# Kernel tuning notes

Hardware: AMD Instinct MI355X
Metric: run time of the kernel (lower is better)

Reference implementation:

```python
import jax, jax.numpy as jnp
import numpy as np

B, L, D, H = 8, 2048, 1024, 2048


def setup_inputs() -> dict:
    key = jax.random.key(0)
    ks = jax.random.split(key, 4)
    hidden = jax.random.normal(ks[0], (B, L, D), dtype=jnp.float32)
    lengths = jax.random.randint(ks[1], (B,), L // 2, L + 1)
    attention_mask = (jnp.arange(L)[None, :] < lengths[:, None]).astype(jnp.float32)
    target_boundary_counts = lengths.astype(jnp.float32) / 8.0
    W1 = jax.random.normal(ks[2], (D, H), dtype=jnp.float32) * (1.0 / np.sqrt(D))
    b1 = jnp.zeros((H,), jnp.float32)
    W2 = jax.random.normal(ks[3], (H, 1), dtype=jnp.float32) * (1.0 / np.sqrt(H))
    b2 = jnp.full((1,), -2.5, jnp.float32)  # init_for_12 bias fill
    return dict(hidden=hidden, attention_mask=attention_mask,
                target_boundary_counts=target_boundary_counts,
                W1=W1, b1=b1, W2=W2, b2=b2)


def sinusoidal_pos_emb(S, d, dtype):
    pos = jnp.arange(S, dtype=jnp.float32)[:, None]
    i = jnp.arange(0, d, 2, dtype=jnp.float32)[None, :]
    ang = pos / jnp.power(10000.0, i / d)
    pe = jnp.zeros((S, d), jnp.float32)
    pe = pe.at[:, 0::2].set(jnp.sin(ang))
    pe = pe.at[:, 1::2].set(jnp.cos(ang))
    return pe.astype(dtype)


def downsample(boundaries, hidden, mask):
    # boundaries: (B,L) straight-through; hidden: (B,L,D); mask: (B,L)
    # segment id of token t = cumsum(b)[t] - b[t]; mean-pool tokens per segment.
    # S is padded to L (static shape); unused trailing segments pool to zero.
    hh1 = jnp.cumsum(boundaries, axis=1) - boundaries            # (B,L)
    foo = jnp.arange(L, dtype=boundaries.dtype)[None, None, :] - hh1[:, :, None]  # (B,L,S)
    sel = jax.lax.stop_gradient(foo) == 0
    lel = jnp.where(sel, 1.0 - foo, 0.0)                          # straight-through weights
    lel = lel * mask[:, :, None]
    lel = lel / (jnp.sum(lel, axis=1, keepdims=True) + 1e-9)
    return jnp.einsum('bld,bls->bsd', hidden, lel)                # (B,S,D)


def reference(hidden, attention_mask, target_boundary_counts, W1, b1, W2, b2):
    # eval mode: dropout is identity, soft_boundaries = probs
    logits = (jax.nn.relu(hidden @ W1 + b1) @ W2 + b2)[..., 0]    # (B,L)
    probs = jax.nn.sigmoid(logits)
    hard = (probs > 0.5).astype(jnp.float32)
    hb = hard + probs - jax.lax.stop_gradient(probs)              # straight-through
    hb = hb * attention_mask
    # force a boundary at the last real token of each padded sequence
    pad = attention_mask == 0
    first_pad = pad & (jnp.cumsum(pad.astype(jnp.int32), axis=1) == 1)
    last_real = jnp.roll(first_pad, -1, axis=1).at[:, -1].set(False)
    hb = jnp.maximum(hb, last_real.astype(jnp.float32))

    pooled = downsample(hb, hidden, attention_mask)               # (B,S=L,D)
    pooled = pooled + sinusoidal_pos_emb(pooled.shape[1], D, pooled.dtype)[None]

    counts = jnp.sum(jax.lax.stop_gradient(hb), axis=1)           # boundaries per item
    shortened_attention_mask = (jnp.arange(L, dtype=jnp.float32)[None, :] < counts[:, None]).astype(jnp.float32)

    # per-item binomial NLL against p = target_count / length, mean over batch, x10
    n = jnp.sum(attention_mask, axis=1)
    k = jnp.sum(hb, axis=1)
    p = jnp.clip(target_boundary_counts / jnp.clip(n, 1.0, None), 1e-6, 1.0 - 1e-6)
    log_prob = (jax.lax.lgamma(n + 1.0) - jax.lax.lgamma(k + 1.0)
                - jax.lax.lgamma(n - k + 1.0)
                + k * jnp.log(p) + (n - k) * jnp.log1p(-p))
    loss = 10.0 * jnp.mean(-log_prob)

    num_boundaries = jnp.sum(hb)
    total_positions = jnp.sum(attention_mask)
    return pooled, loss, num_boundaries, total_positions, shortened_attention_mask
```

## Files before the change

### kernel.cpp

```cpp
#include <hip/hip_runtime.h>
#include <math.h>

#define B_   8
#define L_   2048
#define D_   1024
#define H_   2048
#define NBLK 8
#define CHK  32
#define NCH  (L_ / CHK)
#define BK   64
#define NK   (D_ / BK)
#define MARGIN  0.5f
#define MAXFLAG 1024
#define BSCALE  16.0f
#define BUNSCALE 0.0625f

typedef __bf16 bf16_t;
typedef float  f32x4_t  __attribute__((ext_vector_type(4)));
typedef int    i32x4_t  __attribute__((ext_vector_type(4)));
typedef long   i64x2_t  __attribute__((ext_vector_type(2)));

#define TILE_BYTES 16384

__device__ inline int pk4_fp8(float a, float b, float c, float d) {
  int w = __builtin_amdgcn_cvt_pk_fp8_f32(a, b, 0, false);
  w = __builtin_amdgcn_cvt_pk_fp8_f32(c, d, w, true);
  return w;
}

__global__ __launch_bounds__(256) void k0_pack(
    const float* __restrict__ A,
    const float* __restrict__ W1,
    unsigned char* __restrict__ Abf,
    unsigned char* __restrict__ Bbf,
    float* __restrict__ chunkSum,
    int* __restrict__ flagcnt)
{
  __shared__ float scratch[256][33];
  const int kt = blockIdx.x;
  const int yy = blockIdx.y;
  const int r  = threadIdx.x;

  if (yy >= 64) {
    const int nt = yy - 64;
    if (kt == 0 && nt == 0 && r == 0) *flagcnt = 0;
    const float* src = W1 + (size_t)(kt * BK) * H_ + nt * 256 + r;
    float v[64];
#pragma unroll
    for (int j = 0; j < 64; ++j) v[j] = src[(size_t)j * H_] * BSCALE;
    char* dst = (char*)Bbf + ((size_t)(nt * 16 + kt)) * TILE_BYTES + r * 64;
#pragma unroll
    for (int g = 0; g < 4; ++g) {
      i32x4_t o;
      o[0] = pk4_fp8(v[g*8+0], v[g*8+1], v[g*8+2], v[g*8+3]);
      o[1] = pk4_fp8(v[g*8+4], v[g*8+5], v[g*8+6], v[g*8+7]);
      o[2] = pk4_fp8(v[32+g*8+0], v[32+g*8+1], v[32+g*8+2], v[32+g*8+3]);
      o[3] = pk4_fp8(v[32+g*8+4], v[32+g*8+5], v[32+g*8+6], v[32+g*8+7]);
      *(i32x4_t*)(dst + ((g ^ ((r >> 1) & 3)) << 4)) = o;
    }
    return;
  }

  const int mt = yy;
  const float* src = A + (size_t)(mt * 256 + r) * D_ + kt * BK;
  float v[64];
#pragma unroll
  for (int q = 0; q < 16; ++q) {
    f32x4_t x = *(const f32x4_t*)(src + q * 4);
    v[q*4] = x.x; v[q*4+1] = x.y; v[q*4+2] = x.z; v[q*4+3] = x.w;
  }
  char* dst = (char*)Abf + ((size_t)(mt * 16 + kt)) * TILE_BYTES + r * 64;
#pragma unroll
  for (int g = 0; g < 4; ++g) {
    i32x4_t o;
    o[0] = pk4_fp8(v[g*8+0], v[g*8+1], v[g*8+2], v[g*8+3]);
    o[1] = pk4_fp8(v[g*8+4], v[g*8+5], v[g*8+6], v[g*8+7]);
    o[2] = pk4_fp8(v[32+g*8+0], v[32+g*8+1], v[32+g*8+2], v[32+g*8+3]);
    o[3] = pk4_fp8(v[32+g*8+4], v[32+g*8+5], v[32+g*8+6], v[32+g*8+7]);
    *(i32x4_t*)(dst + ((g ^ ((r >> 1) & 3)) << 4)) = o;
  }
  const int ch = r >> 5, j = r & 31;
  const int b  = mt >> 3;
  const int cg = (mt & 7) * 8 + ch;
#pragma unroll
  for (int half = 0; half < 2; ++half) {
    __syncthreads();
#pragma unroll
    for (int q = 0; q < 8; ++q)
      *(f32x4_t*)&scratch[r][q * 4] = *(const f32x4_t*)&v[half * 32 + q * 4];
    __syncthreads();
    float s = 0.f;
#pragma unroll
    for (int q = 0; q < 32; ++q) s += scratch[ch * 32 + q][j];
    chunkSum[((size_t)(b * NCH + cg)) * D_ + kt * BK + half * 32 + j] = s;
  }
}

__global__ __launch_bounds__(512, 2) void k1_gemm(
    const unsigned char* __restrict__ Abf,
    const unsigned char* __restrict__ Bbf,
    const float* __restrict__ b1,
    const float* __restrict__ W2,
    float* __restrict__ partial)
{
  extern __shared__ __align__(16) unsigned char lds[];

  const int tid  = threadIdx.x;
  const int wg   = (blockIdx.x & 7) * 64 + (blockIdx.x >> 3);
  const int mt   = wg >> 3;
  const int nt   = wg & 7;
  const int m0   = mt * 256;
  const int n0   = nt * 256;
  const int lane = tid & 63;
  const int wave = tid >> 6;
  const int wr = wave >> 2, wc = wave & 3;
  const int lr = lane & 15, lk = lane >> 4;

  const char* aT = (const char*)Abf + ((size_t)mt * NK) * TILE_BYTES;
  const char* bT = (const char*)Bbf + ((size_t)nt * NK) * TILE_BYTES;

  f32x4_t acc[8][4];
#pragma unroll
  for (int m = 0; m < 8; ++m)
#pragma unroll
    for (int n = 0; n < 4; ++n)
      acc[m][n] = (f32x4_t){0.f, 0.f, 0.f, 0.f};

  auto stage = [&](int t, int buf) {
    const char* ga = aT + (size_t)t * TILE_BYTES;
    const char* gb = bT + (size_t)t * TILE_BYTES;
    unsigned char* lb = lds + buf * 32768;
#pragma unroll
    for (int j = 0; j < 4; ++j) {
      const int i = j * 512 + tid;
      const char* g = (j < 2) ? ga + i * 16 : gb + (i - 1024) * 16;
      __builtin_amdgcn_global_load_lds(
          (const __attribute__((address_space(1))) void*)g,
          (__attribute__((address_space(3))) void*)(lb + i * 16),
          16, 0, 0);
    }
  };

  stage(0, 0);
  stage(1, 1);
  for (int t = 0; t < NK; ++t) {
    if (t + 2 < NK) {
      stage(t + 2, (t + 2) & 3);
      asm volatile("s_waitcnt vmcnt(8)" ::: "memory");
    } else if (t + 1 < NK) {
      asm volatile("s_waitcnt vmcnt(4)" ::: "memory");
    } else {
      asm volatile("s_waitcnt vmcnt(0)" ::: "memory");
    }
    __builtin_amdgcn_s_barrier();
    asm volatile("" ::: "memory");

    const char* sA = (const char*)(lds + (t & 3) * 32768);
    const char* sB = sA + 16384;
    i64x2_t a[8], b[4];
#pragma unroll
    for (int m = 0; m < 8; ++m) {
      const int r = wr * 128 + m * 16 + lr;
      a[m] = *(const i64x2_t*)(sA + r * 64 + ((lk ^ ((r >> 1) & 3)) << 4));
    }
#pragma unroll
    for (int n = 0; n < 4; ++n) {
      const int c = wc * 64 + n * 16 + lr;
      b[n] = *(const i64x2_t*)(sB + c * 64 + ((lk ^ ((c >> 1) & 3)) << 4));
    }
#pragma unroll
    for (int m = 0; m < 8; ++m)
#pragma unroll
      for (int n = 0; n < 4; ++n)
        acc[m][n] = __builtin_amdgcn_mfma_f32_16x16x32_fp8_fp8(
            a[m].x, b[n].x, acc[m][n], 0, 0, 0);
#pragma unroll
    for (int m = 0; m < 8; ++m)
#pragma unroll
      for (int n = 0; n < 4; ++n)
        acc[m][n] = __builtin_amdgcn_mfma_f32_16x16x32_fp8_fp8(
            a[m].y, b[n].y, acc[m][n], 0, 0, 0);
  }

  float rs[8][4];
#pragma unroll
  for (int m = 0; m < 8; ++m)
#pragma unroll
    for (int rg = 0; rg < 4; ++rg) rs[m][rg] = 0.f;

#pragma unroll
  for (int n = 0; n < 4; ++n) {
    const int jg = n0 + wc * 64 + n * 16 + lr;
    const float w2v = W2[jg];
    const float b1v = b1[jg];
#pragma unroll
    for (int m = 0; m < 8; ++m)
#pragma unroll
      for (int rg = 0; rg < 4; ++rg) {
        float v = acc[m][n][rg] * BUNSCALE + b1v;
        rs[m][rg] += fmaxf(v, 0.f) * w2v;
      }
  }
#pragma unroll
  for (int m = 0; m < 8; ++m)
#pragma unroll
    for (int rg = 0; rg < 4; ++rg) {
      float v = rs[m][rg];
      v += __shfl_xor(v, 1);
      v += __shfl_xor(v, 2);
      v += __shfl_xor(v, 4);
      v += __shfl_xor(v, 8);
      rs[m][rg] = v;
    }
  __syncthreads();
  float (*part_lds)[4] = (float(*)[4])lds;
  if (lr == 0) {
#pragma unroll
    for (int m = 0; m < 8; ++m)
#pragma unroll
      for (int rg = 0; rg < 4; ++rg)
        part_lds[wr * 128 + m * 16 + lk * 4 + rg][wc] = rs[m][rg];
  }
  __syncthreads();
  if (tid < 256) {
    const float sum = part_lds[tid][0] + part_lds[tid][1]
                    + part_lds[tid][2] + part_lds[tid][3];
    partial[(size_t)(m0 + tid) * NBLK + nt] = sum;
  }
}

__global__ __launch_bounds__(256) void k2a_logits(
    const float* __restrict__ partial,
    const float* __restrict__ b2,
    float* __restrict__ logits,
    int* __restrict__ flaglist,
    int* __restrict__ flagcnt)
{
  const int i = blockIdx.x * 256 + threadIdx.x;
  const float* pp = partial + (size_t)i * NBLK;
  float lg = b2[0];
#pragma unroll
  for (int j = 0; j < NBLK; ++j) lg += pp[j];
  logits[i] = lg;
  if (fabsf(lg) < MARGIN) {
    int s = atomicAdd(flagcnt, 1);
    if (s < MAXFLAG) flaglist[s] = i;
  }
}

__global__ __launch_bounds__(256) void k2b_fixup(
    const float* __restrict__ hidden,
    const float* __restrict__ W1,
    const float* __restrict__ b1,
    const float* __restrict__ W2,
    const int* __restrict__ flaglist,
    const int* __restrict__ flagcnt,
    float* __restrict__ fixpart)
{
  const int cnt = min(*flagcnt, MAXFLAG);
  const int cg = blockIdx.x;
  __shared__ float hrow[D_];
  __shared__ float red[256];
  const int tid = threadIdx.x;
  const int col = cg * 256 + tid;
  for (int f = blockIdx.y; f < cnt; f += 64) {
    const int i = flaglist[f];
    const float* h = hidden + (size_t)i * D_;
    __syncthreads();
    *(f32x4_t*)&hrow[tid * 4] = *(const f32x4_t*)&h[tid * 4];
    __syncthreads();
    float acc = 0.f;
#pragma unroll 8
    for (int k = 0; k < D_; ++k)
      acc = fmaf(hrow[k], W1[(size_t)k * H_ + col], acc);
    red[tid] = fmaxf(acc + b1[col], 0.f) * W2[col];
    __syncthreads();
    for (int st = 128; st > 0; st >>= 1) {
      if (tid < st) red[tid] += red[tid + st];
      __syncthreads();
    }
    if (tid == 0) fixpart[f * 8 + cg] = red[0];
  }
}

__global__ __launch_bounds__(256) void k2c_scan(
    float* __restrict__ logits,
    const float* __restrict__ mask,
    const float* __restrict__ target,
    const float* __restrict__ b2,
    const float* __restrict__ fixpart,
    const int* __restrict__ flaglist,
    const int* __restrict__ flagcnt,
    float* __restrict__ outmask,
    int*   __restrict__ seg,
    float* __restrict__ hdr)
{
  const int b = blockIdx.x, tid = threadIdx.x;
  __shared__ float redf[256];
  __shared__ int tsum[256];
  __shared__ unsigned char hbs[L_];

  const int cnt = min(*flagcnt, MAXFLAG);
  for (int f = tid; f < cnt; f += 256) {
    const int i = flaglist[f];
    if ((i >> 11) == b) {
      float s = b2[0];
#pragma unroll
      for (int cg = 0; cg < 8; ++cg) s += fixpart[f * 8 + cg];
      logits[i] = s;
    }
  }
  float lm = 0.f;
#pragma unroll
  for (int e = 0; e < 8; ++e) lm += mask[b * L_ + tid * 8 + e];
  redf[tid] = lm;
  __syncthreads();
  for (int s = 128; s > 0; s >>= 1) {
    if (tid < s) redf[tid] += redf[tid + s];
    __syncthreads();
  }
  const int length = (int)(redf[0] + 0.5f);

  int hloc[8];
  int lsum = 0;
#pragma unroll
  for (int e = 0; e < 8; ++e) {
    const int t = tid * 8 + e;
    const float lg = logits[b * L_ + t];
    int hb = (lg > 0.f) && (t < length);
    if (length < L_ && t == length - 1) hb = 1;
    hloc[e] = hb;
    hbs[t] = (unsigned char)hb;
    lsum += hb;
  }
  tsum[tid] = lsum;
  __syncthreads();
  for (int off = 1; off < 256; off <<= 1) {
    int v = tsum[tid];
    int add = (tid >= off) ? tsum[tid - off] : 0;
    __syncthreads();
    tsum[tid] = v + add;
    __syncthreads();
  }
  const int ktot = tsum[255];

  int pre = tsum[tid] - lsum;
  for (int e = 0; e < 8; ++e) {
    const int t = tid * 8 + e;
    if (t < length) {
      const bool st = (t == 0) || hbs[t - 1];
      if (st) seg[b * 2050 + pre] = t;
    }
    pre += hloc[e];
  }

#pragma unroll
  for (int e = 0; e < 8; ++e) {
    const int t = tid * 8 + e;
    outmask[b * L_ + t] = (t < ktot) ? 1.f : 0.f;
  }

  __syncthreads();
  if (tid == 0) {
    const int maxseg = ktot - (length > 0 ? (int)hbs[length - 1] : 0);
    seg[b * 2050 + maxseg + 1] = length;
    const float n = (float)length, k = (float)ktot;
    float p = target[b] / fmaxf(n, 1.f);
    p = fminf(fmaxf(p, 1e-6f), 1.f - 1e-6f);
    const float lp = lgammaf(n + 1.f) - lgammaf(k + 1.f) - lgammaf(n - k + 1.f)
                   + k * logf(p) + (n - k) * log1pf(-p);
    hdr[b * 4 + 0] = n;
    hdr[b * 4 + 1] = k;
    hdr[b * 4 + 2] = (float)maxseg;
    hdr[b * 4 + 3] = -lp;
  }
}

__global__ __launch_bounds__(256) void k4b_pool(
    const float* __restrict__ hidden,
    const float* __restrict__ chunkSum,
    const int*   __restrict__ seg,
    const float* __restrict__ hdr,
    float* __restrict__ pooled,
    float* __restrict__ out3)
{
  const int bid = blockIdx.x;
  const int b = bid >> 11, s = bid & 2047;
  const int tid = threadIdx.x;
  if (bid == 0 && tid == 0) {
    float s_lp = 0.f, s_k = 0.f, s_n = 0.f;
    for (int i = 0; i < B_; ++i) {
      s_n  += hdr[i * 4 + 0];
      s_k  += hdr[i * 4 + 1];
      s_lp += hdr[i * 4 + 3];
    }
    out3[0] = 10.f * (s_lp * 0.125f);
    out3[1] = s_k;
    out3[2] = s_n;
  }
  const int maxseg = (int)hdr[b * 4 + 2];

  float a0 = 0.f, a1 = 0.f, a2 = 0.f, a3 = 0.f;
  if (s <= maxseg) {
    const int st = seg[b * 2050 + s];
    const int en = seg[b * 2050 + s + 1];
    const float* hrow = hidden + (size_t)(b * L_) * D_ + tid * 4;
    const float* crow = chunkSum + (size_t)(b * NCH) * D_ + tid * 4;
    const int cs = (st + CHK - 1) / CHK;
    const int ce = en / CHK;
    if (cs >= ce) {
      for (int t = st; t < en; ++t) {
        const f32x4_t v = *(const f32x4_t*)(hrow + (size_t)t * D_);
        a0 += v.x; a1 += v.y; a2 += v.z; a3 += v.w;
      }
    } else {
      for (int t = st; t < cs * CHK; ++t) {
        const f32x4_t v = *(const f32x4_t*)(hrow + (size_t)t * D_);
        a0 += v.x; a1 += v.y; a2 += v.z; a3 += v.w;
      }
#pragma unroll 4
      for (int c = cs; c < ce; ++c) {
        const f32x4_t v = *(const f32x4_t*)(crow + (size_t)c * D_);
        a0 += v.x; a1 += v.y; a2 += v.z; a3 += v.w;
      }
      for (int t = ce * CHK; t < en; ++t) {
        const f32x4_t v = *(const f32x4_t*)(hrow + (size_t)t * D_);
        a0 += v.x; a1 += v.y; a2 += v.z; a3 += v.w;
      }
    }
    const float cnt = (float)(en - st);
    const float inv = 1.f / (cnt + 1e-9f);
    a0 *= inv; a1 *= inv; a2 *= inv; a3 *= inv;
  }
  const float L2_10K = 13.287712379549449f;
  const float e0 = (float)(4 * tid)     * (1.f / 1024.f);
  const float e1 = (float)(4 * tid + 2) * (1.f / 1024.f);
  const float ang0 = (float)s * exp2f(-e0 * L2_10K);
  const float ang1 = (float)s * exp2f(-e1 * L2_10K);
  float s0, c0, s1, c1;
  __sincosf(ang0, &s0, &c0);
  __sincosf(ang1, &s1, &c1);
  f32x4_t o;
  o.x = a0 + s0; o.y = a1 + c0; o.z = a2 + s1; o.w = a3 + c1;
  *(f32x4_t*)(pooled + ((size_t)(b * L_ + s)) * D_ + tid * 4) = o;
}

extern "C" void kernel_launch(void* const* d_in, const int* in_sizes, int n_in,
                              void* d_out, int out_size, void* d_ws, size_t ws_size,
                              hipStream_t stream)
{
  (void)in_sizes; (void)n_in; (void)out_size; (void)ws_size;
  const float* hidden = (const float*)d_in[0];
  const float* amask  = (const float*)d_in[1];
  const float* target = (const float*)d_in[2];
  const float* W1     = (const float*)d_in[3];
  const float* b1     = (const float*)d_in[4];
  const float* W2     = (const float*)d_in[5];
  const float* b2     = (const float*)d_in[6];

  float* out     = (float*)d_out;
  float* pooled  = out;
  float* out3    = out + 16777216;
  float* outmask = out + 16777219;

  unsigned char* Abf = (unsigned char*)out;
  unsigned char* Bbf = (unsigned char*)(out + 8388608);

  char* ws = (char*)d_ws;
  float* partial  = (float*)ws;                      ws += (size_t)16384 * NBLK * 4;
  int*   seg      = (int*)ws;                        ws += (size_t)B_ * 2050 * 4;
  float* hdr      = (float*)ws;                      ws += (size_t)B_ * 4 * 4;
  float* logits   = (float*)ws;                      ws += (size_t)B_ * L_ * 4;
  int*   flaglist = (int*)ws;                        ws += (size_t)MAXFLAG * 4;
  int*   flagcnt  = (int*)ws;                        ws += 256;
  float* fixpart  = (float*)ws;                      ws += (size_t)MAXFLAG * 8 * 4;
  float* chunkSum = (float*)ws;

  k0_pack<<<dim3(NK, 72), dim3(256), 0, stream>>>(hidden, W1, Abf, Bbf,
                                                  chunkSum, flagcnt);
  k1_gemm<<<dim3(512), dim3(512), 131072, stream>>>(Abf, Bbf, b1, W2, partial);
  k2a_logits<<<dim3(64), dim3(256), 0, stream>>>(partial, b2, logits, flaglist, flagcnt);
  k2b_fixup<<<dim3(8, 64), dim3(256), 0, stream>>>(hidden, W1, b1, W2,
                                                   flaglist, flagcnt, fixpart);
  k2c_scan<<<dim3(8), dim3(256), 0, stream>>>(logits, amask, target, b2, fixpart,
                                              flaglist, flagcnt, outmask, seg, hdr);
  k4b_pool<<<dim3(16384), dim3(256), 0, stream>>>(hidden, chunkSum, seg, hdr, pooled, out3);
}
```

Baseline: 107.4 us.

## Use MI355 scaled fp8 16x16x128 MFMA with BK=128 double-buffered tiles

Switches the fp8 GEMM from 16x16x32 MFMAs to the gfx950 scaled 16x16x128 f8f6f4 MFMA with unit scales, doubling the K tile to 128 and changing the packed tile layout and swizzle to match. The LDS pipeline drops from a 4-buffer, two-stage-ahead prefetch to double buffering with an extra barrier per iteration. The pack kernel is rewritten for the new layout. This cuts MFMA instruction count and loop iterations, but there is less prefetch depth and each stage uses more LDS (128KB total), which may limit occupancy and the (512,2) launch bound.

```diff
diff --git a/kernel.cpp b/kernel.cpp
--- a/kernel.cpp
+++ b/kernel.cpp
@@ -8,19 +8,18 @@
 #define NBLK 8
 #define CHK  32
 #define NCH  (L_ / CHK)
-#define BK   64
+#define BK   128
 #define NK   (D_ / BK)
 #define MARGIN  0.5f
 #define MAXFLAG 1024
 #define BSCALE  16.0f
 #define BUNSCALE 0.0625f
 
-typedef __bf16 bf16_t;
 typedef float  f32x4_t  __attribute__((ext_vector_type(4)));
 typedef int    i32x4_t  __attribute__((ext_vector_type(4)));
-typedef long   i64x2_t  __attribute__((ext_vector_type(2)));
-
-#define TILE_BYTES 16384
+typedef int    i32x8_t  __attribute__((ext_vector_type(8)));
+
+#define TILE_BYTES 32768
 
 __device__ inline int pk4_fp8(float a, float b, float c, float d) {
   int w = __builtin_amdgcn_cvt_pk_fp8_f32(a, b, 0, false);
@@ -45,54 +44,63 @@
     const int nt = yy - 64;
     if (kt == 0 && nt == 0 && r == 0) *flagcnt = 0;
     const float* src = W1 + (size_t)(kt * BK) * H_ + nt * 256 + r;
-    float v[64];
-#pragma unroll
-    for (int j = 0; j < 64; ++j) v[j] = src[(size_t)j * H_] * BSCALE;
-    char* dst = (char*)Bbf + ((size_t)(nt * 16 + kt)) * TILE_BYTES + r * 64;
-#pragma unroll
-    for (int g = 0; g < 4; ++g) {
-      i32x4_t o;
-      o[0] = pk4_fp8(v[g*8+0], v[g*8+1], v[g*8+2], v[g*8+3]);
-      o[1] = pk4_fp8(v[g*8+4], v[g*8+5], v[g*8+6], v[g*8+7]);
-      o[2] = pk4_fp8(v[32+g*8+0], v[32+g*8+1], v[32+g*8+2], v[32+g*8+3]);
-      o[3] = pk4_fp8(v[32+g*8+4], v[32+g*8+5], v[32+g*8+6], v[32+g*8+7]);
-      *(i32x4_t*)(dst + ((g ^ ((r >> 1) & 3)) << 4)) = o;
+    char* dst = (char*)Bbf + ((size_t)(nt * 8 + kt)) * TILE_BYTES + r * 128;
+#pragma unroll
+    for (int h = 0; h < 2; ++h) {
+      float v[64];
+#pragma unroll
+      for (int j = 0; j < 64; ++j)
+        v[j] = src[(size_t)(h * 64 + j) * H_] * BSCALE;
+#pragma unroll
+      for (int q = 0; q < 4; ++q) {
+        const int c = h * 4 + q;
+        i32x4_t o;
+        o[0] = pk4_fp8(v[q*16+ 0], v[q*16+ 1], v[q*16+ 2], v[q*16+ 3]);
+        o[1] = pk4_fp8(v[q*16+ 4], v[q*16+ 5], v[q*16+ 6], v[q*16+ 7]);
+        o[2] = pk4_fp8(v[q*16+ 8], v[q*16+ 9], v[q*16+10], v[q*16+11]);
+        o[3] = pk4_fp8(v[q*16+12], v[q*16+13], v[q*16+14], v[q*16+15]);
+        *(i32x4_t*)(dst + ((c ^ (r & 7)) << 4)) = o;
+      }
     }
     return;
   }
 
   const int mt = yy;
   const float* src = A + (size_t)(mt * 256 + r) * D_ + kt * BK;
-  float v[64];
-#pragma unroll
-  for (int q = 0; q < 16; ++q) {
-    f32x4_t x = *(const f32x4_t*)(src + q * 4);
-    v[q*4] = x.x; v[q*4+1] = x.y; v[q*4+2] = x.z; v[q*4+3] = x.w;
-  }
-  char* dst = (char*)Abf + ((size_t)(mt * 16 + kt)) * TILE_BYTES + r * 64;
-#pragma unroll
-  for (int g = 0; g < 4; ++g) {
-    i32x4_t o;
-    o[0] = pk4_fp8(v[g*8+0], v[g*8+1], v[g*8+2], v[g*8+3]);
-    o[1] = pk4_fp8(v[g*8+4], v[g*8+5], v[g*8+6], v[g*8+7]);
-    o[2] = pk4_fp8(v[32+g*8+0], v[32+g*8+1], v[32+g*8+2], v[32+g*8+3]);
-    o[3] = pk4_fp8(v[32+g*8+4], v[32+g*8+5], v[32+g*8+6], v[32+g*8+7]);
-    *(i32x4_t*)(dst + ((g ^ ((r >> 1) & 3)) << 4)) = o;
-  }
+  char* dst = (char*)Abf + ((size_t)(mt * 8 + kt)) * TILE_BYTES + r * 128;
   const int ch = r >> 5, j = r & 31;
   const int b  = mt >> 3;
   const int cg = (mt & 7) * 8 + ch;
 #pragma unroll
-  for (int half = 0; half < 2; ++half) {
-    __syncthreads();
-#pragma unroll
-    for (int q = 0; q < 8; ++q)
-      *(f32x4_t*)&scratch[r][q * 4] = *(const f32x4_t*)&v[half * 32 + q * 4];
-    __syncthreads();
-    float s = 0.f;
-#pragma unroll
-    for (int q = 0; q < 32; ++q) s += scratch[ch * 32 + q][j];
-    chunkSum[((size_t)(b * NCH + cg)) * D_ + kt * BK + half * 32 + j] = s;
+  for (int h = 0; h < 2; ++h) {
+    float v[64];
+#pragma unroll
+    for (int q = 0; q < 16; ++q) {
+      f32x4_t x = *(const f32x4_t*)(src + h * 64 + q * 4);
+      v[q*4] = x.x; v[q*4+1] = x.y; v[q*4+2] = x.z; v[q*4+3] = x.w;
+    }
+#pragma unroll
+    for (int q = 0; q < 4; ++q) {
+      const int c = h * 4 + q;
+      i32x4_t o;
+      o[0] = pk4_fp8(v[q*16+ 0], v[q*16+ 1], v[q*16+ 2], v[q*16+ 3]);
+      o[1] = pk4_fp8(v[q*16+ 4], v[q*16+ 5], v[q*16+ 6], v[q*16+ 7]);
+      o[2] = pk4_fp8(v[q*16+ 8], v[q*16+ 9], v[q*16+10], v[q*16+11]);
+      o[3] = pk4_fp8(v[q*16+12], v[q*16+13], v[q*16+14], v[q*16+15]);
+      *(i32x4_t*)(dst + ((c ^ (r & 7)) << 4)) = o;
+    }
+#pragma unroll
+    for (int sub = 0; sub < 2; ++sub) {
+      __syncthreads();
+#pragma unroll
+      for (int q = 0; q < 8; ++q)
+        *(f32x4_t*)&scratch[r][q * 4] = *(const f32x4_t*)&v[sub * 32 + q * 4];
+      __syncthreads();
+      float s = 0.f;
+#pragma unroll
+      for (int q = 0; q < 32; ++q) s += scratch[ch * 32 + q][j];
+      chunkSum[((size_t)(b * NCH + cg)) * D_ + kt * BK + h * 64 + sub * 32 + j] = s;
+    }
   }
 }
 
@@ -129,11 +137,11 @@
   auto stage = [&](int t, int buf) {
     const char* ga = aT + (size_t)t * TILE_BYTES;
     const char* gb = bT + (size_t)t * TILE_BYTES;
-    unsigned char* lb = lds + buf * 32768;
-#pragma unroll
-    for (int j = 0; j < 4; ++j) {
-      const int i = j * 512 + tid;
-      const char* g = (j < 2) ? ga + i * 16 : gb + (i - 1024) * 16;
+    unsigned char* lb = lds + buf * 65536;
+#pragma unroll
+    for (int jj = 0; jj < 8; ++jj) {
+      const int i = jj * 512 + tid;
+      const char* g = (jj < 4) ? ga + i * 16 : gb + (i - 2048) * 16;
       __builtin_amdgcn_global_load_lds(
           (const __attribute__((address_space(1))) void*)g,
           (__attribute__((address_space(3))) void*)(lb + i * 16),
@@ -142,44 +150,51 @@
   };
 
   stage(0, 0);
-  stage(1, 1);
   for (int t = 0; t < NK; ++t) {
-    if (t + 2 < NK) {
-      stage(t + 2, (t + 2) & 3);
+    __builtin_amdgcn_s_barrier();
+    if (t + 1 < NK) {
+      stage(t + 1, (t + 1) & 1);
       asm volatile("s_waitcnt vmcnt(8)" ::: "memory");
-    } else if (t + 1 < NK) {
-      asm volatile("s_waitcnt vmcnt(4)" ::: "memory");
     } else {
       asm volatile("s_waitcnt vmcnt(0)" ::: "memory");
     }
     __builtin_amdgcn_s_barrier();
     asm volatile("" ::: "memory");
 
-    const char* sA = (const char*)(lds + (t & 3) * 32768);
-    const char* sB = sA + 16384;
-    i64x2_t a[8], b[4];
-#pragma unroll
-    for (int m = 0; m < 8; ++m) {
-      const int r = wr * 128 + m * 16 + lr;
-      a[m] = *(const i64x2_t*)(sA + r * 64 + ((lk ^ ((r >> 1) & 3)) << 4));
-    }
+    const char* sA = (const char*)(lds + (t & 1) * 65536);
+    const char* sB = sA + 32768;
+
+    i32x8_t bfr[4];
 #pragma unroll
     for (int n = 0; n < 4; ++n) {
       const int c = wc * 64 + n * 16 + lr;
-      b[n] = *(const i64x2_t*)(sB + c * 64 + ((lk ^ ((c >> 1) & 3)) << 4));
-    }
-#pragma unroll
-    for (int m = 0; m < 8; ++m)
-#pragma unroll
-      for (int n = 0; n < 4; ++n)
-        acc[m][n] = __builtin_amdgcn_mfma_f32_16x16x32_fp8_fp8(
-            a[m].x, b[n].x, acc[m][n], 0, 0, 0);
-#pragma unroll
-    for (int m = 0; m < 8; ++m)
-#pragma unroll
-      for (int n = 0; n < 4; ++n)
-        acc[m][n] = __builtin_amdgcn_mfma_f32_16x16x32_fp8_fp8(
-            a[m].y, b[n].y, acc[m][n], 0, 0, 0);
+      const char* base = sB + c * 128;
+      i32x4_t lo = *(const i32x4_t*)(base + (((2 * lk)     ^ (c & 7)) << 4));
+      i32x4_t hi = *(const i32x4_t*)(base + (((2 * lk + 1) ^ (c & 7)) << 4));
+      bfr[n][0] = lo[0]; bfr[n][1] = lo[1]; bfr[n][2] = lo[2]; bfr[n][3] = lo[3];
+      bfr[n][4] = hi[0]; bfr[n][5] = hi[1]; bfr[n][6] = hi[2]; bfr[n][7] = hi[3];
+    }
+#pragma unroll
+    for (int mh = 0; mh < 2; ++mh) {
+      i32x8_t afr[4];
+#pragma unroll
+      for (int i = 0; i < 4; ++i) {
+        const int rr = wr * 128 + (mh * 4 + i) * 16 + lr;
+        const char* base = sA + rr * 128;
+        i32x4_t lo = *(const i32x4_t*)(base + (((2 * lk)     ^ (rr & 7)) << 4));
+        i32x4_t hi = *(const i32x4_t*)(base + (((2 * lk + 1) ^ (rr & 7)) << 4));
+        afr[i][0] = lo[0]; afr[i][1] = lo[1]; afr[i][2] = lo[2]; afr[i][3] = lo[3];
+        afr[i][4] = hi[0]; afr[i][5] = hi[1]; afr[i][6] = hi[2]; afr[i][7] = hi[3];
+      }
+#pragma unroll
+      for (int i = 0; i < 4; ++i)
+#pragma unroll
+        for (int n = 0; n < 4; ++n)
+          acc[mh * 4 + i][n] = __builtin_amdgcn_mfma_scale_f32_16x16x128_f8f6f4(
+              afr[i], bfr[n], acc[mh * 4 + i][n],
+              0 , 0 ,
+              0, 127 , 0, 127 );
+    }
   }
 
   float rs[8][4];
```

Result: faster. 100.1 us (-6.8%).
